# Performance work log

Measured on AMD Instinct MI355X. Metric: run time of the kernel, lower is better.

Reference implementation:

```python
import jax, jax.numpy as jnp
import numpy as np

DIMS = 2048
Q_HEADS = 32
K_HEADS = 8
HEAD_DIM = DIMS // Q_HEADS  # 64
KV_DIM = K_HEADS * HEAD_DIM  # 512
B, S, IN_DIM = 2, 2048, 2048


def setup_inputs() -> dict:
    key = jax.random.key(0)
    ks = jax.random.split(key, 11)
    sc_in = 1.0 / np.sqrt(IN_DIM)
    sc_out = 1.0 / np.sqrt(DIMS)
    return {
        "q": jax.random.normal(ks[0], (B, S, IN_DIM), jnp.float32),
        "k": jax.random.normal(ks[1], (B, S, IN_DIM), jnp.float32),
        "v": jax.random.normal(ks[2], (B, S, IN_DIM), jnp.float32),
        "Wq": jax.random.normal(ks[3], (IN_DIM, DIMS), jnp.float32) * sc_in,
        "bq": jnp.zeros((DIMS,), jnp.float32),
        "Wk": jax.random.normal(ks[4], (IN_DIM, KV_DIM), jnp.float32) * sc_in,
        "bk": jnp.zeros((KV_DIM,), jnp.float32),
        "Wv": jax.random.normal(ks[5], (IN_DIM, KV_DIM), jnp.float32) * sc_in,
        "bv": jnp.zeros((KV_DIM,), jnp.float32),
        "Wo": jax.random.normal(ks[6], (DIMS, IN_DIM), jnp.float32) * sc_out,
        "bo": jnp.zeros((IN_DIM,), jnp.float32),
    }


def reference(q, k, v, Wq, bq, Wk, bk, Wv, bv, Wo, bo):
    rep = Q_HEADS // K_HEADS
    # projections
    qx = (q @ Wq + bq).reshape(B, S, Q_HEADS, HEAD_DIM)
    kx = (k @ Wk + bk).reshape(B, S, K_HEADS, HEAD_DIM)
    vx = (v @ Wv + bv).reshape(B, S, K_HEADS, HEAD_DIM)
    # repeat kv heads to match q heads (matches kx.repeat(rep, axis=-2))
    kx = jnp.repeat(kx, rep, axis=-2)
    vx = jnpp_repeat(vx, rep) if False else jnp.repeat(vx, rep, axis=-2)
    # [B, H, S, D]
    qx = jnp.einsum('bshd->bhsd', qx)
    kx = jnp.einsum('bshd->bhsd', kx)
    vx = jnp.einsum('bshd->bhsd', vx)
    scores = jnp.einsum('bhqd,bhkd->bhqk', qx, kx) / jnp.sqrt(
        jnp.asarray(HEAD_DIM, qx.dtype))
    scores = jax.nn.softmax(scores, axis=-1)
    out = jnp.einsum('bhqk,bhkd->bhqd', scores, vx)
    out = jnp.einsum('bhsd->bshd', out).reshape(B, S, DIMS)
    return out @ Wo + bo
```

## Files before the change

### kernel.cpp

```cpp
#include <hip/hip_runtime.h>
#include <cstdint>
#include <cstddef>

typedef _Float16 half8   __attribute__((ext_vector_type(8)));
typedef _Float16 half4_t __attribute__((ext_vector_type(4)));
typedef __fp16   fp16x2  __attribute__((ext_vector_type(2)));
typedef float    f32x4   __attribute__((ext_vector_type(4)));

typedef __attribute__((address_space(1))) const void GV;
typedef __attribute__((address_space(3))) void LV;

__device__ __forceinline__ void gl_lds16(const _Float16* g, _Float16* l) {
    __builtin_amdgcn_global_load_lds((GV*)g, (LV*)l, 16, 0, 0);
}

#define BB    2
#define SS    2048
#define INDIM 2048
#define DIMS_ 2048
#define QH    32
#define KH_   8
#define HD    64
#define KVD   512
#define RWS   4096

#define QSCALE (0.125f * 1.44269504088896340736f)

__global__ void cast_f16_3(const float* __restrict__ a, const float* __restrict__ b,
                           const float* __restrict__ c,
                           _Float16* __restrict__ oa, _Float16* __restrict__ ob,
                           _Float16* __restrict__ oc) {
    const float* in  = (blockIdx.y == 0) ? a : (blockIdx.y == 1) ? b : c;
    _Float16*    out = (blockIdx.y == 0) ? oa : (blockIdx.y == 1) ? ob : oc;
    int i = (blockIdx.x * 256 + threadIdx.x) * 8;
    const float4* p = (const float4*)(in + i);
    float4 x = p[0], y = p[1];
    half8 h;
    h[0]=(_Float16)x.x; h[1]=(_Float16)x.y; h[2]=(_Float16)x.z; h[3]=(_Float16)x.w;
    h[4]=(_Float16)y.x; h[5]=(_Float16)y.y; h[6]=(_Float16)y.z; h[7]=(_Float16)y.w;
    *(half8*)(out + i) = h;
}

__global__ void transpose_cast4(const float* __restrict__ in0, _Float16* __restrict__ out0,
                                const float* __restrict__ in1, _Float16* __restrict__ out1,
                                const float* __restrict__ in2, _Float16* __restrict__ out2,
                                const float* __restrict__ in3, _Float16* __restrict__ out3,
                                int R, int C01, int C23) {
    const int z = blockIdx.z;
    const float* in; _Float16* out; int C;
    if (z == 0)      { in = in0; out = out0; C = C01; }
    else if (z == 1) { in = in1; out = out1; C = C01; }
    else if (z == 2) { in = in2; out = out2; C = C23; }
    else             { in = in3; out = out3; C = C23; }
    int c0 = blockIdx.x * 32;
    if (c0 >= C) return;
    __shared__ float t[32][33];
    int r0 = blockIdx.y * 32;
    int tx = threadIdx.x, ty = threadIdx.y;
    for (int i = ty; i < 32; i += 8)
        t[i][tx] = in[(size_t)(r0 + i) * C + c0 + tx];
    __syncthreads();
    for (int i = ty; i < 32; i += 8)
        out[(size_t)(c0 + i) * R + r0 + tx] = (_Float16)t[tx][i];
}

__global__ __launch_bounds__(256) void gemm_qkv(
    const _Float16* __restrict__ q16, const _Float16* __restrict__ k16,
    const _Float16* __restrict__ v16,
    const _Float16* __restrict__ WqT, const _Float16* __restrict__ WkT,
    const _Float16* __restrict__ WvT,
    const float* __restrict__ bq, const float* __restrict__ bk,
    const float* __restrict__ bv,
    _Float16* __restrict__ qx, _Float16* __restrict__ kx,
    _Float16* __restrict__ vtg)
{
    const int bid = blockIdx.x;
    const _Float16* A; const _Float16* Bt; const float* bias;
    int bn, bm, N, mode; float scale;
    if (bid < 512)      { mode = 0; A = q16; Bt = WqT; bias = bq; N = 2048;
                          bn = bid & 15; bm = bid >> 4; scale = QSCALE; }
    else if (bid < 640) { int t = bid - 512; mode = 1; A = k16; Bt = WkT; bias = bk;
                          N = 512; bn = t & 3; bm = t >> 2; scale = 1.0f; }
    else                { int t = bid - 640; mode = 2; A = v16; Bt = WvT; bias = bv;
                          N = 512; bn = t & 3; bm = t >> 2; scale = 1.0f; }
    const int K = 2048;

    const int tid = threadIdx.x;
    const int wave = tid >> 6, lane = tid & 63, quad = lane >> 4, l15 = lane & 15;
    const int wm = wave & 1, wn = wave >> 1;

    __shared__ __align__(16) _Float16 As[128 * 32];
    __shared__ __align__(16) _Float16 Bs[128 * 32];

    f32x4 acc[4][4] = {};

    for (int kt = 0; kt < K / 32; ++kt) {
        __syncthreads();
        const _Float16* Ag = A  + (size_t)(bm * 128) * K + kt * 32;
        const _Float16* Bg = Bt + (size_t)(bn * 128) * K + kt * 32;
#pragma unroll
        for (int i = 0; i < 2; ++i) {
            int f = i * 256 + tid;
            gl_lds16(Ag + (size_t)(f >> 2) * K + (f & 3) * 8,
                     As + (size_t)(i * 256 + (tid & 192)) * 8);
            gl_lds16(Bg + (size_t)(f >> 2) * K + (f & 3) * 8,
                     Bs + (size_t)(i * 256 + (tid & 192)) * 8);
        }
        __syncthreads();

        half8 af[4], bf[4];
#pragma unroll
        for (int i = 0; i < 4; ++i)
            af[i] = *(const half8*)(As + (wm * 64 + i * 16 + l15) * 32 + quad * 8);
#pragma unroll
        for (int j = 0; j < 4; ++j)
            bf[j] = *(const half8*)(Bs + (wn * 64 + j * 16 + l15) * 32 + quad * 8);
#pragma unroll
        for (int i = 0; i < 4; ++i)
#pragma unroll
            for (int j = 0; j < 4; ++j)
                acc[i][j] = __builtin_amdgcn_mfma_f32_16x16x32_f16(af[i], bf[j], acc[i][j], 0, 0, 0);
    }

    const int row0 = bm * 128 + wm * 64;
    const int col0 = bn * 128 + wn * 64;
    if (mode < 2) {
        _Float16* out = mode ? kx : qx;
#pragma unroll
        for (int j = 0; j < 4; ++j) {
            int col = col0 + j * 16 + l15;
            float bv_ = bias[col];
#pragma unroll
            for (int i = 0; i < 4; ++i)
#pragma unroll
                for (int r = 0; r < 4; ++r) {
                    int row = row0 + i * 16 + quad * 4 + r;
                    out[(size_t)row * N + col] = (_Float16)((acc[i][j][r] + bv_) * scale);
                }
        }
    } else {
#pragma unroll
        for (int j = 0; j < 4; ++j) {
            int c = col0 + j * 16 + l15;
            int kh = c >> 6, d = c & 63;
            float bv_ = bias[c];
#pragma unroll
            for (int i = 0; i < 4; ++i) {
                int row = row0 + i * 16 + quad * 4;
                int bb2 = row >> 11, s = row & 2047;
                half4_t hp;
#pragma unroll
                for (int r = 0; r < 4; ++r) hp[r] = (_Float16)(acc[i][j][r] + bv_);
                *(half4_t*)(vtg + ((size_t)(bb2 * KH_ + kh) * HD + d) * SS + s) = hp;
            }
        }
    }
}

__global__ __launch_bounds__(256) void gemm_oproj(
    const _Float16* __restrict__ A, const _Float16* __restrict__ Bt,
    const float* __restrict__ bias, float* __restrict__ Cf)
{
    const int N = 2048, K = 2048;
    const int bn = blockIdx.x, bm = blockIdx.y;
    const int tid = threadIdx.x;
    const int wave = tid >> 6, lane = tid & 63, quad = lane >> 4, l15 = lane & 15;
    const int wm = wave & 1, wn = wave >> 1;

    __shared__ __align__(16) _Float16 As[128 * 32];
    __shared__ __align__(16) _Float16 Bs[128 * 32];

    f32x4 acc[4][4] = {};

    for (int kt = 0; kt < K / 32; ++kt) {
        __syncthreads();
        const _Float16* Ag = A  + (size_t)(bm * 128) * K + kt * 32;
        const _Float16* Bg = Bt + (size_t)(bn * 128) * K + kt * 32;
#pragma unroll
        for (int i = 0; i < 2; ++i) {
            int f = i * 256 + tid;
            gl_lds16(Ag + (size_t)(f >> 2) * K + (f & 3) * 8,
                     As + (size_t)(i * 256 + (tid & 192)) * 8);
            gl_lds16(Bg + (size_t)(f >> 2) * K + (f & 3) * 8,
                     Bs + (size_t)(i * 256 + (tid & 192)) * 8);
        }
        __syncthreads();

        half8 af[4], bf[4];
#pragma unroll
        for (int i = 0; i < 4; ++i)
            af[i] = *(const half8*)(As + (wm * 64 + i * 16 + l15) * 32 + quad * 8);
#pragma unroll
        for (int j = 0; j < 4; ++j)
            bf[j] = *(const half8*)(Bs + (wn * 64 + j * 16 + l15) * 32 + quad * 8);
#pragma unroll
        for (int i = 0; i < 4; ++i)
#pragma unroll
            for (int j = 0; j < 4; ++j)
                acc[i][j] = __builtin_amdgcn_mfma_f32_16x16x32_f16(af[i], bf[j], acc[i][j], 0, 0, 0);
    }

    const int row0 = bm * 128 + wm * 64;
    const int col0 = bn * 128 + wn * 64;
#pragma unroll
    for (int j = 0; j < 4; ++j) {
        int col = col0 + j * 16 + l15;
        float bv_ = bias[col];
#pragma unroll
        for (int i = 0; i < 4; ++i)
#pragma unroll
            for (int r = 0; r < 4; ++r) {
                int row = row0 + i * 16 + quad * 4 + r;
                Cf[(size_t)row * N + col] = acc[i][j][r] + bv_;
            }
    }
}

__global__ __launch_bounds__(256, 2) void attn_fused(
    const _Float16* __restrict__ qx, const _Float16* __restrict__ kx,
    const _Float16* __restrict__ vt, _Float16* __restrict__ o16)
{
    const int qt = blockIdx.x;
    const int bh = blockIdx.y;
    const int bb = bh >> 5, h = bh & 31, kh = h >> 2;
    const int tid = threadIdx.x;
    const int w = tid >> 6, lane = tid & 63, quad = lane >> 4, l15 = lane & 15;

    __shared__ __align__(16) _Float16 Ks[2][64 * 64];
    __shared__ __align__(16) _Float16 Vs[2][64 * 64];
    __shared__ __align__(16) _Float16 Ps[4][64 * 72];

    const size_t qrow0 = (size_t)bb * SS + (size_t)qt * 256 + w * 64;
    half8 qf[4][2];
#pragma unroll
    for (int nb = 0; nb < 4; ++nb)
#pragma unroll
        for (int kk = 0; kk < 2; ++kk)
            qf[nb][kk] = *(const half8*)(qx + (qrow0 + nb * 16 + l15) * DIMS_
                                            + h * HD + kk * 32 + quad * 8);

    half8 vone;
#pragma unroll
    for (int i = 0; i < 8; ++i) vone[i] = (_Float16)1.0f;

    f32x4 ob[4][4] = {};
    f32x4 lacc[4] = {};

    const _Float16* kbase = kx + (size_t)bb * SS * KVD + kh * HD;
    const _Float16* vbase = vt + (size_t)(bb * KH_ + kh) * HD * SS;
    _Float16* Pw = &Ps[w][0];

    const int srowlo = lane >> 3;
    const int scol   = ((lane & 7) ^ srowlo) * 8;

#pragma unroll
    for (int i = 0; i < 2; ++i) {
        int row = w * 16 + i * 8 + srowlo;
        gl_lds16(kbase + (size_t)row * KVD + scol,
                 &Ks[0][0] + (w * 16 + i * 8) * 64);
        gl_lds16(vbase + (size_t)row * SS + scol,
                 &Vs[0][0] + (w * 16 + i * 8) * 64);
    }

    for (int kt = 0; kt < SS / 64; ++kt) {
        const int cur = kt & 1;
        if (kt < SS / 64 - 1) {
            const int nx = cur ^ 1;
#pragma unroll
            for (int i = 0; i < 2; ++i) {
                int row = w * 16 + i * 8 + srowlo;
                gl_lds16(kbase + (size_t)((kt + 1) * 64 + row) * KVD + scol,
                         &Ks[nx][0] + (w * 16 + i * 8) * 64);
                gl_lds16(vbase + (size_t)row * SS + (kt + 1) * 64 + scol,
                         &Vs[nx][0] + (w * 16 + i * 8) * 64);
            }
            asm volatile("s_waitcnt vmcnt(4)" ::: "memory");
        } else {
            asm volatile("s_waitcnt vmcnt(0)" ::: "memory");
        }
        __builtin_amdgcn_s_barrier();

        const _Float16* Kc = &Ks[cur][0];
        const _Float16* Vc = &Vs[cur][0];

#pragma unroll
        for (int mk = 0; mk < 4; ++mk) {
            f32x4 st4[4] = {};
#pragma unroll
            for (int kk = 0; kk < 2; ++kk) {
                half8 ka = *(const half8*)(Kc + (mk * 16 + l15) * 64
                                              + (((kk * 4 + quad) ^ (l15 & 7)) * 8));
                __builtin_amdgcn_s_setprio(1);
#pragma unroll
                for (int nb = 0; nb < 4; ++nb)
                    st4[nb] = __builtin_amdgcn_mfma_f32_16x16x32_f16(
                        ka, qf[nb][kk], st4[nb], 0, 0, 0);
                __builtin_amdgcn_s_setprio(0);
            }
#pragma unroll
            for (int nb = 0; nb < 4; ++nb) {
                float p0 = __builtin_amdgcn_exp2f(st4[nb][0]);
                float p1 = __builtin_amdgcn_exp2f(st4[nb][1]);
                float p2 = __builtin_amdgcn_exp2f(st4[nb][2]);
                float p3 = __builtin_amdgcn_exp2f(st4[nb][3]);
                fp16x2 lo = __builtin_amdgcn_cvt_pkrtz(p0, p1);
                fp16x2 hi = __builtin_amdgcn_cvt_pkrtz(p2, p3);
                half4_t hp;
                hp[0] = (_Float16)lo[0]; hp[1] = (_Float16)lo[1];
                hp[2] = (_Float16)hi[0]; hp[3] = (_Float16)hi[1];
                *(half4_t*)(Pw + (nb * 16 + l15) * 72 + mk * 16 + quad * 4) = hp;
            }
        }

#pragma unroll
        for (int kk = 0; kk < 2; ++kk) {
            half8 pa[4], vb[4];
#pragma unroll
            for (int mb = 0; mb < 4; ++mb)
                pa[mb] = *(const half8*)(Pw + (mb * 16 + l15) * 72 + kk * 32 + quad * 8);
#pragma unroll
            for (int nd = 0; nd < 4; ++nd)
                vb[nd] = *(const half8*)(Vc + (nd * 16 + l15) * 64
                                            + (((kk * 4 + quad) ^ (l15 & 7)) * 8));
            __builtin_amdgcn_s_setprio(1);
#pragma unroll
            for (int mb = 0; mb < 4; ++mb) {
#pragma unroll
                for (int nd = 0; nd < 4; ++nd)
                    ob[mb][nd] = __builtin_amdgcn_mfma_f32_16x16x32_f16(
                        pa[mb], vb[nd], ob[mb][nd], 0, 0, 0);
                lacc[mb] = __builtin_amdgcn_mfma_f32_16x16x32_f16(
                    pa[mb], vone, lacc[mb], 0, 0, 0);
            }
            __builtin_amdgcn_s_setprio(0);
        }
        __builtin_amdgcn_s_barrier();
    }

#pragma unroll
    for (int mb = 0; mb < 4; ++mb)
#pragma unroll
        for (int r = 0; r < 4; ++r) {
            float rl = __builtin_amdgcn_rcpf(lacc[mb][r]);
            size_t row = qrow0 + mb * 16 + quad * 4 + r;
#pragma unroll
            for (int nd = 0; nd < 4; ++nd)
                o16[row * DIMS_ + h * HD + nd * 16 + l15] =
                    (_Float16)(ob[mb][nd][r] * rl);
        }
}

extern "C" void kernel_launch(void* const* d_in, const int* in_sizes, int n_in,
                              void* d_out, int out_size, void* d_ws, size_t ws_size,
                              hipStream_t stream) {
    const float* q  = (const float*)d_in[0];
    const float* k  = (const float*)d_in[1];
    const float* v  = (const float*)d_in[2];
    const float* Wq = (const float*)d_in[3];
    const float* bq = (const float*)d_in[4];
    const float* Wk = (const float*)d_in[5];
    const float* bk = (const float*)d_in[6];
    const float* Wv = (const float*)d_in[7];
    const float* bv = (const float*)d_in[8];
    const float* Wo = (const float*)d_in[9];
    const float* bo = (const float*)d_in[10];

    char* ws = (char*)d_ws;
    _Float16* q16  = (_Float16*)ws;  ws += (size_t)RWS * INDIM * 2;
    _Float16* k16  = (_Float16*)ws;  ws += (size_t)RWS * INDIM * 2;
    _Float16* v16  = (_Float16*)ws;  ws += (size_t)RWS * INDIM * 2;
    _Float16* qx16 = (_Float16*)ws;  ws += (size_t)RWS * DIMS_ * 2;
    _Float16* kx16 = (_Float16*)ws;  ws += (size_t)RWS * KVD * 2;
    _Float16* o16  = (_Float16*)ws;  ws += (size_t)RWS * DIMS_ * 2;
    _Float16* WqT  = (_Float16*)ws;  ws += (size_t)DIMS_ * INDIM * 2;
    _Float16* WkT  = (_Float16*)ws;  ws += (size_t)KVD * INDIM * 2;
    _Float16* WvT  = (_Float16*)ws;  ws += (size_t)KVD * INDIM * 2;
    _Float16* WoT  = (_Float16*)ws;  ws += (size_t)INDIM * DIMS_ * 2;
    _Float16* vtg  = (_Float16*)ws;  ws += (size_t)BB * KH_ * HD * SS * 2;

    const int nAct = RWS * INDIM;
    cast_f16_3<<<dim3(nAct / (256 * 8), 3), 256, 0, stream>>>(q, k, v, q16, k16, v16);

    transpose_cast4<<<dim3(DIMS_ / 32, INDIM / 32, 4), dim3(32, 8), 0, stream>>>(
        Wq, WqT, Wo, WoT, Wk, WkT, Wv, WvT, INDIM, DIMS_, KVD);

    gemm_qkv<<<768, 256, 0, stream>>>(q16, k16, v16, WqT, WkT, WvT,
                                      bq, bk, bv, qx16, kx16, vtg);

    attn_fused<<<dim3(SS / 256, BB * QH), 256, 0, stream>>>(qx16, kx16, vtg, o16);

    gemm_oproj<<<dim3(INDIM / 128, RWS / 128), 256, 0, stream>>>(
        o16, WoT, bo, (float*)d_out);
}
```

Measured before the change: 379.3 us.

## Double-buffer GEMM LDS loads; shrink attention tile to 128 rows for occupancy

Both projection GEMMs now double-buffer their A/B tiles in LDS. The next k-tile is issued with global_load_lds before computing on the current one, and MFMA runs at raised priority. The attention kernel goes the other way: its K/V double buffering is removed, each block covers 128 query rows instead of 256, and launch bounds ask for 4 blocks per CU. This trades attention load latency hiding and per-block K/V reuse for more resident blocks and more parallelism, while the GEMMs gain load/compute overlap at the cost of twice the LDS.

```diff
diff --git a/kernel.cpp b/kernel.cpp
--- a/kernel.cpp
+++ b/kernel.cpp
@@ -89,37 +89,57 @@
     const int wave = tid >> 6, lane = tid & 63, quad = lane >> 4, l15 = lane & 15;
     const int wm = wave & 1, wn = wave >> 1;
 
-    __shared__ __align__(16) _Float16 As[128 * 32];
-    __shared__ __align__(16) _Float16 Bs[128 * 32];
+    __shared__ __align__(16) _Float16 As[2][128 * 32];
+    __shared__ __align__(16) _Float16 Bs[2][128 * 32];
 
     f32x4 acc[4][4] = {};
 
+    const _Float16* Agb = A  + (size_t)(bm * 128) * K;
+    const _Float16* Bgb = Bt + (size_t)(bn * 128) * K;
+
+#define QKV_STAGE(T, BUF)                                                     \
+    {                                                                         \
+        const _Float16* Ag = Agb + (T) * 32;                                  \
+        const _Float16* Bg = Bgb + (T) * 32;                                  \
+        _Float16* Ad = &As[BUF][0];                                           \
+        _Float16* Bd = &Bs[BUF][0];                                           \
+        _Pragma("unroll")                                                     \
+        for (int i_ = 0; i_ < 2; ++i_) {                                      \
+            int f_ = i_ * 256 + tid;                                          \
+            gl_lds16(Ag + (size_t)(f_ >> 2) * K + (f_ & 3) * 8,               \
+                     Ad + (size_t)(i_ * 256 + (tid & 192)) * 8);              \
+            gl_lds16(Bg + (size_t)(f_ >> 2) * K + (f_ & 3) * 8,               \
+                     Bd + (size_t)(i_ * 256 + (tid & 192)) * 8);              \
+        }                                                                     \
+    }
+
+    QKV_STAGE(0, 0);
+
     for (int kt = 0; kt < K / 32; ++kt) {
-        __syncthreads();
-        const _Float16* Ag = A  + (size_t)(bm * 128) * K + kt * 32;
-        const _Float16* Bg = Bt + (size_t)(bn * 128) * K + kt * 32;
-#pragma unroll
-        for (int i = 0; i < 2; ++i) {
-            int f = i * 256 + tid;
-            gl_lds16(Ag + (size_t)(f >> 2) * K + (f & 3) * 8,
-                     As + (size_t)(i * 256 + (tid & 192)) * 8);
-            gl_lds16(Bg + (size_t)(f >> 2) * K + (f & 3) * 8,
-                     Bs + (size_t)(i * 256 + (tid & 192)) * 8);
-        }
-        __syncthreads();
+        const int cur = kt & 1;
+        if (kt < K / 32 - 1) {
+            QKV_STAGE(kt + 1, cur ^ 1);
+            asm volatile("s_waitcnt vmcnt(4)" ::: "memory");
+        } else {
+            asm volatile("s_waitcnt vmcnt(0)" ::: "memory");
+        }
+        __builtin_amdgcn_s_barrier();
 
         half8 af[4], bf[4];
 #pragma unroll
         for (int i = 0; i < 4; ++i)
-            af[i] = *(const half8*)(As + (wm * 64 + i * 16 + l15) * 32 + quad * 8);
+            af[i] = *(const half8*)(&As[cur][0] + (wm * 64 + i * 16 + l15) * 32 + quad * 8);
 #pragma unroll
         for (int j = 0; j < 4; ++j)
-            bf[j] = *(const half8*)(Bs + (wn * 64 + j * 16 + l15) * 32 + quad * 8);
+            bf[j] = *(const half8*)(&Bs[cur][0] + (wn * 64 + j * 16 + l15) * 32 + quad * 8);
+        __builtin_amdgcn_s_setprio(1);
 #pragma unroll
         for (int i = 0; i < 4; ++i)
 #pragma unroll
             for (int j = 0; j < 4; ++j)
                 acc[i][j] = __builtin_amdgcn_mfma_f32_16x16x32_f16(af[i], bf[j], acc[i][j], 0, 0, 0);
+        __builtin_amdgcn_s_setprio(0);
+        __builtin_amdgcn_s_barrier();
     }
 
     const int row0 = bm * 128 + wm * 64;
@@ -167,37 +187,41 @@
     const int wave = tid >> 6, lane = tid & 63, quad = lane >> 4, l15 = lane & 15;
     const int wm = wave & 1, wn = wave >> 1;
 
-    __shared__ __align__(16) _Float16 As[128 * 32];
-    __shared__ __align__(16) _Float16 Bs[128 * 32];
+    __shared__ __align__(16) _Float16 As[2][128 * 32];
+    __shared__ __align__(16) _Float16 Bs[2][128 * 32];
 
     f32x4 acc[4][4] = {};
 
+    const _Float16* Agb = A  + (size_t)(bm * 128) * K;
+    const _Float16* Bgb = Bt + (size_t)(bn * 128) * K;
+
+    QKV_STAGE(0, 0);
+
     for (int kt = 0; kt < K / 32; ++kt) {
-        __syncthreads();
-        const _Float16* Ag = A  + (size_t)(bm * 128) * K + kt * 32;
-        const _Float16* Bg = Bt + (size_t)(bn * 128) * K + kt * 32;
-#pragma unroll
-        for (int i = 0; i < 2; ++i) {
-            int f = i * 256 + tid;
-            gl_lds16(Ag + (size_t)(f >> 2) * K + (f & 3) * 8,
-                     As + (size_t)(i * 256 + (tid & 192)) * 8);
-            gl_lds16(Bg + (size_t)(f >> 2) * K + (f & 3) * 8,
-                     Bs + (size_t)(i * 256 + (tid & 192)) * 8);
-        }
-        __syncthreads();
+        const int cur = kt & 1;
+        if (kt < K / 32 - 1) {
+            QKV_STAGE(kt + 1, cur ^ 1);
+            asm volatile("s_waitcnt vmcnt(4)" ::: "memory");
+        } else {
+            asm volatile("s_waitcnt vmcnt(0)" ::: "memory");
+        }
+        __builtin_amdgcn_s_barrier();
 
         half8 af[4], bf[4];
 #pragma unroll
         for (int i = 0; i < 4; ++i)
-            af[i] = *(const half8*)(As + (wm * 64 + i * 16 + l15) * 32 + quad * 8);
+            af[i] = *(const half8*)(&As[cur][0] + (wm * 64 + i * 16 + l15) * 32 + quad * 8);
 #pragma unroll
         for (int j = 0; j < 4; ++j)
-            bf[j] = *(const half8*)(Bs + (wn * 64 + j * 16 + l15) * 32 + quad * 8);
+            bf[j] = *(const half8*)(&Bs[cur][0] + (wn * 64 + j * 16 + l15) * 32 + quad * 8);
+        __builtin_amdgcn_s_setprio(1);
 #pragma unroll
         for (int i = 0; i < 4; ++i)
 #pragma unroll
             for (int j = 0; j < 4; ++j)
                 acc[i][j] = __builtin_amdgcn_mfma_f32_16x16x32_f16(af[i], bf[j], acc[i][j], 0, 0, 0);
+        __builtin_amdgcn_s_setprio(0);
+        __builtin_amdgcn_s_barrier();
     }
 
     const int row0 = bm * 128 + wm * 64;
@@ -216,7 +240,7 @@
     }
 }
 
-__global__ __launch_bounds__(256, 2) void attn_fused(
+__global__ __launch_bounds__(256, 4) void attn_fused(
     const _Float16* __restrict__ qx, const _Float16* __restrict__ kx,
     const _Float16* __restrict__ vt, _Float16* __restrict__ o16)
 {
@@ -226,14 +250,14 @@
     const int tid = threadIdx.x;
     const int w = tid >> 6, lane = tid & 63, quad = lane >> 4, l15 = lane & 15;
 
-    __shared__ __align__(16) _Float16 Ks[2][64 * 64];
-    __shared__ __align__(16) _Float16 Vs[2][64 * 64];
-    __shared__ __align__(16) _Float16 Ps[4][64 * 72];
-
-    const size_t qrow0 = (size_t)bb * SS + (size_t)qt * 256 + w * 64;
-    half8 qf[4][2];
-#pragma unroll
-    for (int nb = 0; nb < 4; ++nb)
+    __shared__ __align__(16) _Float16 Ks[64 * 64];
+    __shared__ __align__(16) _Float16 Vs[64 * 64];
+    __shared__ __align__(16) _Float16 Ps[4][32 * 72];
+
+    const size_t qrow0 = (size_t)bb * SS + (size_t)qt * 128 + w * 32;
+    half8 qf[2][2];
+#pragma unroll
+    for (int nb = 0; nb < 2; ++nb)
 #pragma unroll
         for (int kk = 0; kk < 2; ++kk)
             qf[nb][kk] = *(const half8*)(qx + (qrow0 + nb * 16 + l15) * DIMS_
@@ -243,8 +267,8 @@
 #pragma unroll
     for (int i = 0; i < 8; ++i) vone[i] = (_Float16)1.0f;
 
-    f32x4 ob[4][4] = {};
-    f32x4 lacc[4] = {};
+    f32x4 ob[2][4] = {};
+    f32x4 lacc[2] = {};
 
     const _Float16* kbase = kx + (size_t)bb * SS * KVD + kh * HD;
     const _Float16* vbase = vt + (size_t)(bb * KH_ + kh) * HD * SS;
@@ -253,52 +277,34 @@
     const int srowlo = lane >> 3;
     const int scol   = ((lane & 7) ^ srowlo) * 8;
 
-#pragma unroll
-    for (int i = 0; i < 2; ++i) {
-        int row = w * 16 + i * 8 + srowlo;
-        gl_lds16(kbase + (size_t)row * KVD + scol,
-                 &Ks[0][0] + (w * 16 + i * 8) * 64);
-        gl_lds16(vbase + (size_t)row * SS + scol,
-                 &Vs[0][0] + (w * 16 + i * 8) * 64);
-    }
-
     for (int kt = 0; kt < SS / 64; ++kt) {
-        const int cur = kt & 1;
-        if (kt < SS / 64 - 1) {
-            const int nx = cur ^ 1;
-#pragma unroll
-            for (int i = 0; i < 2; ++i) {
-                int row = w * 16 + i * 8 + srowlo;
-                gl_lds16(kbase + (size_t)((kt + 1) * 64 + row) * KVD + scol,
-                         &Ks[nx][0] + (w * 16 + i * 8) * 64);
-                gl_lds16(vbase + (size_t)row * SS + (kt + 1) * 64 + scol,
-                         &Vs[nx][0] + (w * 16 + i * 8) * 64);
-            }
-            asm volatile("s_waitcnt vmcnt(4)" ::: "memory");
-        } else {
-            asm volatile("s_waitcnt vmcnt(0)" ::: "memory");
-        }
-        __builtin_amdgcn_s_barrier();
-
-        const _Float16* Kc = &Ks[cur][0];
-        const _Float16* Vc = &Vs[cur][0];
+        __syncthreads();
+#pragma unroll
+        for (int i = 0; i < 2; ++i) {
+            int row = w * 16 + i * 8 + srowlo;
+            gl_lds16(kbase + (size_t)(kt * 64 + row) * KVD + scol,
+                     Ks + (w * 16 + i * 8) * 64);
+            gl_lds16(vbase + (size_t)row * SS + kt * 64 + scol,
+                     Vs + (w * 16 + i * 8) * 64);
+        }
+        __syncthreads();
 
 #pragma unroll
         for (int mk = 0; mk < 4; ++mk) {
-            f32x4 st4[4] = {};
+            f32x4 st4[2] = {};
 #pragma unroll
             for (int kk = 0; kk < 2; ++kk) {
-                half8 ka = *(const half8*)(Kc + (mk * 16 + l15) * 64
+                half8 ka = *(const half8*)(Ks + (mk * 16 + l15) * 64
                                               + (((kk * 4 + quad) ^ (l15 & 7)) * 8));
                 __builtin_amdgcn_s_setprio(1);
 #pragma unroll
-                for (int nb = 0; nb < 4; ++nb)
+                for (int nb = 0; nb < 2; ++nb)
                     st4[nb] = __builtin_amdgcn_mfma_f32_16x16x32_f16(
                         ka, qf[nb][kk], st4[nb], 0, 0, 0);
                 __builtin_amdgcn_s_setprio(0);
             }
 #pragma unroll
-            for (int nb = 0; nb < 4; ++nb) {
+            for (int nb = 0; nb < 2; ++nb) {
                 float p0 = __builtin_amdgcn_exp2f(st4[nb][0]);
                 float p1 = __builtin_amdgcn_exp2f(st4[nb][1]);
                 float p2 = __builtin_amdgcn_exp2f(st4[nb][2]);
@@ -314,17 +320,17 @@
 
 #pragma unroll
         for (int kk = 0; kk < 2; ++kk) {
-            half8 pa[4], vb[4];
-#pragma unroll
-            for (int mb = 0; mb < 4; ++mb)
+            half8 pa[2], vb[4];
+#pragma unroll
+            for (int mb = 0; mb < 2; ++mb)
                 pa[mb] = *(const half8*)(Pw + (mb * 16 + l15) * 72 + kk * 32 + quad * 8);
 #pragma unroll
             for (int nd = 0; nd < 4; ++nd)
-                vb[nd] = *(const half8*)(Vc + (nd * 16 + l15) * 64
+                vb[nd] = *(const half8*)(Vs + (nd * 16 + l15) * 64
                                             + (((kk * 4 + quad) ^ (l15 & 7)) * 8));
             __builtin_amdgcn_s_setprio(1);
 #pragma unroll
-            for (int mb = 0; mb < 4; ++mb) {
+            for (int mb = 0; mb < 2; ++mb) {
 #pragma unroll
                 for (int nd = 0; nd < 4; ++nd)
                     ob[mb][nd] = __builtin_amdgcn_mfma_f32_16x16x32_f16(
@@ -334,11 +340,10 @@
             }
             __builtin_amdgcn_s_setprio(0);
         }
-        __builtin_amdgcn_s_barrier();
-    }
-
-#pragma unroll
-    for (int mb = 0; mb < 4; ++mb)
+    }
+
+#pragma unroll
+    for (int mb = 0; mb < 2; ++mb)
 #pragma unroll
         for (int r = 0; r < 4; ++r) {
             float rl = __builtin_amdgcn_rcpf(lacc[mb][r]);
@@ -387,7 +392,7 @@
     gemm_qkv<<<768, 256, 0, stream>>>(q16, k16, v16, WqT, WkT, WvT,
                                       bq, bk, bv, qx16, kx16, vtg);
 
-    attn_fused<<<dim3(SS / 256, BB * QH), 256, 0, stream>>>(qx16, kx16, vtg, o16);
+    attn_fused<<<dim3(SS / 128, BB * QH), 256, 0, stream>>>(qx16, kx16, vtg, o16);
 
     gemm_oproj<<<dim3(INDIM / 128, RWS / 128), 256, 0, stream>>>(
         o16, WoT, bo, (float*)d_out);
```

New measurement: 404.3 us. 1.07x slower.
